# Optimization experiments

Hardware: AMD Instinct MI355X
Metric: run time of the kernel (lower is better)

The kernel has to match this reference:

```python
import jax, jax.numpy as jnp
import numpy as np

# alpha clamp limits: balance=False -> [exp(-1/5), exp(-1/25)]
ALPHA_MIN = float(np.exp(-1.0 / 5.0))
ALPHA_MAX = float(np.exp(-1.0 / 25.0))
T_CROP = 100


def setup_inputs() -> dict:
    key = jax.random.key(0)
    k1, k2, k3 = jax.random.split(key, 3)
    B, T, D, H = 128, 1000, 1024, 256
    x = jax.random.normal(k1, (B, T, D), dtype=jnp.float32)
    bound = float(np.sqrt(1.0 / D))
    W = jax.random.uniform(k2, (H, D), minval=-bound, maxval=bound, dtype=jnp.float32)
    alpha = jax.random.uniform(k3, (H,), minval=ALPHA_MIN, maxval=ALPHA_MAX, dtype=jnp.float32)
    return {"x": x, "W": W, "alpha": alpha}


def reference(x, W, alpha):
    # x: [B, T, D], W: [H, D], alpha: [H]
    a = jnp.clip(alpha, ALPHA_MIN, ALPHA_MAX)
    Wx = jnp.einsum('btd,hd->bth', x, W)  # [B, T, H]
    T = Wx.shape[1]
    mask = (jnp.arange(T) >= T_CROP).astype(Wx.dtype)  # [T]
    Wx_t = jnp.moveaxis(Wx, 1, 0)  # [T, B, H]

    def step(carry, inp):
        ut, out = carry
        wx, m = inp
        ut = a * ut + (1.0 - a) * wx
        out = out + m * jax.nn.softmax(ut, axis=-1)
        return (ut, out), None

    B, H = Wx.shape[0], Wx.shape[2]
    init = (jnp.zeros((B, H), Wx.dtype), jnp.zeros((B, H), Wx.dtype))
    (_, out), _ = jax.lax.scan(step, init, (Wx_t, mask))
    return out  # [B, H]
```

## Files before the change

### kernel.cpp

```cpp
#include <hip/hip_runtime.h>
#include <hip/hip_bf16.h>

#define B_    128
#define T_    1000
#define D_    1024
#define H_    256
#define TCROP 100
#define CHK   125
#define NC    8
#define NOUT  900

typedef __attribute__((ext_vector_type(8))) short bfrag8;
typedef __attribute__((ext_vector_type(4))) float f32x4;
typedef unsigned long long ull;

__device__ __forceinline__ unsigned short f2bf(float f) {
    union { float f; unsigned int u; } v; v.f = f;
    unsigned int u = v.u;
    u += 0x7FFFu + ((u >> 16) & 1u);
    return (unsigned short)(u >> 16);
}
__device__ __forceinline__ float bf2f(unsigned short u) {
    union { unsigned int u; float f; } v; v.u = ((unsigned int)u) << 16;
    return v.f;
}
__device__ __forceinline__ bfrag8 cvt8(float4 f0, float4 f1) {
    bfrag8 v;
    v[0] = (short)f2bf(f0.x); v[1] = (short)f2bf(f0.y);
    v[2] = (short)f2bf(f0.z); v[3] = (short)f2bf(f0.w);
    v[4] = (short)f2bf(f1.x); v[5] = (short)f2bf(f1.y);
    v[6] = (short)f2bf(f1.z); v[7] = (short)f2bf(f1.w);
    return v;
}

__global__ __launch_bounds__(256) void wconv_kernel(
        const float* __restrict__ W, unsigned short* __restrict__ Wbf) {
    const int i = (blockIdx.x * 256 + threadIdx.x) * 8;
    float4 f0 = *(const float4*)(W + i);
    float4 f1 = *(const float4*)(W + i + 4);
    *(bfrag8*)(Wbf + i) = cvt8(f0, f1);
}

__global__ __launch_bounds__(512) void gemm_ema_kernel(
        const float* __restrict__ x, const unsigned short* __restrict__ Wbf,
        const float* __restrict__ alpha,
        unsigned short* __restrict__ utl, float* __restrict__ F) {
    __shared__ unsigned short smem[128 * 256];
    unsigned short* As = smem;
    unsigned short* Bs = smem + 128 * 64;

    const int tid  = threadIdx.x;
    const int lane = tid & 63;
    const int wave = tid >> 6;
    const int wr   = wave >> 2;
    const int wc   = wave & 3;
    const int c    = blockIdx.x;
    const int b    = blockIdx.y;
    const int m0   = b * T_ + c * CHK;

    f32x4 acc[4][4];
#pragma unroll
    for (int m = 0; m < 4; ++m)
#pragma unroll
        for (int n = 0; n < 4; ++n) acc[m][n] = (f32x4){0.f, 0.f, 0.f, 0.f};

    const int rr  = lane & 15;
    const int kh  = lane >> 4;
    const int ra0 = tid >> 3;
    const int ja  = tid & 7;
    const int sa  = (ja ^ (ra0 & 7)) * 8;
    const int rA1 = (ra0 + 64 < CHK) ? (ra0 + 64) : (CHK - 1);
    const float* ap0 = x + (size_t)(m0 + ra0) * D_ + ja * 8;
    const float* ap1 = x + (size_t)(m0 + rA1) * D_ + ja * 8;

    float4 p00 = *(const float4*)ap0;
    float4 p01 = *(const float4*)(ap0 + 4);
    float4 p10 = *(const float4*)ap1;
    float4 p11 = *(const float4*)(ap1 + 4);

    for (int it = 0; it < 16; ++it) {
        const int kt = it * 64;
#pragma unroll
        for (int q = 0; q < 4; ++q) {
            const int li = q * 512 + tid;
            const int r = li >> 3, j = li & 7;
            const int jj = j ^ (r & 7);
            __builtin_amdgcn_global_load_lds(
                (const __attribute__((address_space(1))) void*)
                    (Wbf + (size_t)r * D_ + kt + jj * 8),
                (__attribute__((address_space(3))) void*)&Bs[li * 8], 16, 0, 0);
        }
        *(bfrag8*)&As[ra0 * 64 + sa]        = cvt8(p00, p01);
        *(bfrag8*)&As[(ra0 + 64) * 64 + sa] = cvt8(p10, p11);
        __syncthreads();
        if (it < 15) {
            const int ktn = kt + 64;
            p00 = *(const float4*)(ap0 + ktn);
            p01 = *(const float4*)(ap0 + ktn + 4);
            p10 = *(const float4*)(ap1 + ktn);
            p11 = *(const float4*)(ap1 + ktn + 4);
        }
#pragma unroll
        for (int kk = 0; kk < 2; ++kk) {
            const int c16 = kk * 4 + kh;
            bfrag8 af[4], bfr[4];
#pragma unroll
            for (int m = 0; m < 4; ++m) {
                const int row = wr * 64 + m * 16 + rr;
                af[m] = *(const bfrag8*)&As[row * 64 + ((c16 ^ (row & 7)) * 8)];
            }
#pragma unroll
            for (int n = 0; n < 4; ++n) {
                const int row = wc * 64 + n * 16 + rr;
                bfr[n] = *(const bfrag8*)&Bs[row * 64 + ((c16 ^ (row & 7)) * 8)];
            }
#pragma unroll
            for (int m = 0; m < 4; ++m)
#pragma unroll
                for (int n = 0; n < 4; ++n)
                    acc[m][n] = __builtin_amdgcn_mfma_f32_16x16x32_bf16(
                        af[m], bfr[n], acc[m][n], 0, 0, 0);
        }
        __syncthreads();
    }

    const int cl = lane & 15, rg = lane >> 4;
#pragma unroll
    for (int m = 0; m < 4; ++m)
#pragma unroll
        for (int n = 0; n < 4; ++n)
#pragma unroll
            for (int j = 0; j < 4; ++j) {
                const int row = wr * 64 + m * 16 + rg * 4 + j;
                const int col = (wc * 64 + n * 16 + cl + rg * 16) & 255;
                smem[row * 256 + col] = f2bf(acc[m][n][j]);
            }
    __syncthreads();

    if (tid < H_) {
        const int h = tid;
        const float AMIN = 0.81873075307798182f, AMAX = 0.96078943915232320f;
        const float a  = fminf(fmaxf(alpha[h], AMIN), AMAX);
        const float om = 1.0f - a;
        float ut = 0.f;
        const int t0 = c * CHK;
        for (int r = 0; r < CHK; ++r) {
            const int col = (h + ((r >> 2) & 3) * 16) & 255;
            ut = a * ut + om * bf2f(smem[r * 256 + col]);
            const int t = t0 + r;
            if (t >= TCROP)
                utl[((size_t)b * NOUT + (t - TCROP)) * H_ + h] = f2bf(ut);
        }
        F[((size_t)b * NC + c) * H_ + h] = ut;
    }
}

__global__ __launch_bounds__(64) void scanC_kernel(
        const unsigned short* __restrict__ utl, const float* __restrict__ alpha,
        const float* __restrict__ F, float* __restrict__ P) {
    const int c = blockIdx.x, b = blockIdx.y;
    const int lane = threadIdx.x;
    const int h4 = lane * 4;

    const float AMIN = 0.81873075307798182f, AMAX = 0.96078943915232320f;
    float4 al = *(const float4*)(alpha + h4);
    float a[4] = {fminf(fmaxf(al.x, AMIN), AMAX), fminf(fmaxf(al.y, AMIN), AMAX),
                  fminf(fmaxf(al.z, AMIN), AMAX), fminf(fmaxf(al.w, AMIN), AMAX)};

    float S[4] = {0.f, 0.f, 0.f, 0.f};
    if (c > 0) {
        float aL[4] = {__powf(a[0], (float)CHK), __powf(a[1], (float)CHK),
                       __powf(a[2], (float)CHK), __powf(a[3], (float)CHK)};
        for (int j = 0; j < c; ++j) {
            float4 f = *(const float4*)(F + ((size_t)b * NC + j) * H_ + h4);
            S[0] = aL[0] * S[0] + f.x;
            S[1] = aL[1] * S[1] + f.y;
            S[2] = aL[2] * S[2] + f.z;
            S[3] = aL[3] * S[3] + f.w;
        }
    }

    const int nt = (c == 0) ? (CHK - TCROP) : CHK;
    const size_t ti0 = (size_t)b * NOUT + (c == 0 ? 0 : c * CHK - TCROP);
    const unsigned short* base = utl + ti0 * H_ + h4;

    float d[4]    = {1.f, 1.f, 1.f, 1.f};
    float acc4[4] = {0.f, 0.f, 0.f, 0.f};

    for (int bb = 0; bb < nt; bb += 5) {
        float e[5][4], sl[5];
#pragma unroll
        for (int q = 0; q < 5; ++q) {
            ull wv = *(const ull*)(base + (size_t)(bb + q) * H_);
            d[0] *= a[0]; d[1] *= a[1]; d[2] *= a[2]; d[3] *= a[3];
            float u0 = bf2f((unsigned short)wv)         + d[0] * S[0];
            float u1 = bf2f((unsigned short)(wv >> 16)) + d[1] * S[1];
            float u2 = bf2f((unsigned short)(wv >> 32)) + d[2] * S[2];
            float u3 = bf2f((unsigned short)(wv >> 48)) + d[3] * S[3];
            e[q][0] = __expf(u0);
            e[q][1] = __expf(u1);
            e[q][2] = __expf(u2);
            e[q][3] = __expf(u3);
            sl[q] = (e[q][0] + e[q][1]) + (e[q][2] + e[q][3]);
        }
#pragma unroll
        for (int dd = 1; dd < 64; dd <<= 1) {
            sl[0] += __shfl_xor(sl[0], dd);
            sl[1] += __shfl_xor(sl[1], dd);
            sl[2] += __shfl_xor(sl[2], dd);
            sl[3] += __shfl_xor(sl[3], dd);
            sl[4] += __shfl_xor(sl[4], dd);
        }
#pragma unroll
        for (int q = 0; q < 5; ++q) {
            const float rcp = 1.0f / sl[q];
            acc4[0] += e[q][0] * rcp;
            acc4[1] += e[q][1] * rcp;
            acc4[2] += e[q][2] * rcp;
            acc4[3] += e[q][3] * rcp;
        }
    }
    float4 o; o.x = acc4[0]; o.y = acc4[1]; o.z = acc4[2]; o.w = acc4[3];
    *(float4*)(P + ((size_t)b * NC + c) * H_ + h4) = o;
}

__global__ __launch_bounds__(256) void scanD_kernel(
        const float* __restrict__ P, float* __restrict__ out) {
    const int b = blockIdx.x, h = threadIdx.x;
    float s = 0.f;
#pragma unroll
    for (int c = 0; c < NC; ++c) s += P[((size_t)b * NC + c) * H_ + h];
    out[(size_t)b * H_ + h] = s;
}

extern "C" void kernel_launch(void* const* d_in, const int* in_sizes, int n_in,
                              void* d_out, int out_size, void* d_ws, size_t ws_size,
                              hipStream_t stream) {
    const float* x     = (const float*)d_in[0];
    const float* W     = (const float*)d_in[1];
    const float* alpha = (const float*)d_in[2];
    float* out = (float*)d_out;

    char* ws = (char*)d_ws;
    unsigned short* Wbf = (unsigned short*)ws;
    unsigned short* utl = (unsigned short*)(ws + ((size_t)1 << 20));
    float* F = (float*)(ws + ((size_t)64 << 20));
    float* P = (float*)(ws + ((size_t)66 << 20));

    wconv_kernel<<<128, 256, 0, stream>>>(W, Wbf);
    gemm_ema_kernel<<<dim3(NC, B_), 512, 0, stream>>>(x, Wbf, alpha, utl, F);
    scanC_kernel<<<dim3(NC, B_), 64, 0, stream>>>(utl, alpha, F, P);
    scanD_kernel<<<B_, 256, 0, stream>>>(P, out);
}
```

Measured before the change: 205.3 us.

## Split GEMM from EMA scan and use finer 25-step chunks for scan parallelism

The GEMM no longer fuses the per-chunk EMA. It tiles the flattened B*T rows densely in 128-row blocks with no padded rows and writes Wx in bf16. Two new scan passes follow: one computes per-chunk EMA end states over 40 chunks of 25 steps, and one carries the prefix into each chunk, recomputing the EMA and summing softmax only for chunks past the crop. This spreads the serial recurrence across many more waves, at the cost of an extra Wx round trip and recomputing the EMA. The bf16 conversion also switches to a perm-based pack with round-half-up rounding.

```diff
diff --git a/kernel.cpp b/kernel.cpp
--- a/kernel.cpp
+++ b/kernel.cpp
@@ -6,9 +6,10 @@
 #define D_    1024
 #define H_    256
 #define TCROP 100
-#define CHK   125
-#define NC    8
-#define NOUT  900
+#define CHUNK 25
+#define NCHK  40
+#define CSKIP 4
+#define NOUTC 36
 
 typedef __attribute__((ext_vector_type(8))) short bfrag8;
 typedef __attribute__((ext_vector_type(4))) float f32x4;
@@ -24,13 +25,17 @@
     union { unsigned int u; float f; } v; v.u = ((unsigned int)u) << 16;
     return v.f;
 }
+__device__ __forceinline__ unsigned int pack2(float lo, float hi) {
+    union { float f; unsigned int u; } a, b; a.f = lo; b.f = hi;
+    return __builtin_amdgcn_perm(b.u + 0x8000u, a.u + 0x8000u, 0x07060302u);
+}
 __device__ __forceinline__ bfrag8 cvt8(float4 f0, float4 f1) {
-    bfrag8 v;
-    v[0] = (short)f2bf(f0.x); v[1] = (short)f2bf(f0.y);
-    v[2] = (short)f2bf(f0.z); v[3] = (short)f2bf(f0.w);
-    v[4] = (short)f2bf(f1.x); v[5] = (short)f2bf(f1.y);
-    v[6] = (short)f2bf(f1.z); v[7] = (short)f2bf(f1.w);
-    return v;
+    union { bfrag8 v; unsigned int u[4]; } r;
+    r.u[0] = pack2(f0.x, f0.y);
+    r.u[1] = pack2(f0.z, f0.w);
+    r.u[2] = pack2(f1.x, f1.y);
+    r.u[3] = pack2(f1.z, f1.w);
+    return r.v;
 }
 
 __global__ __launch_bounds__(256) void wconv_kernel(
@@ -41,22 +46,18 @@
     *(bfrag8*)(Wbf + i) = cvt8(f0, f1);
 }
 
-__global__ __launch_bounds__(512) void gemm_ema_kernel(
+__global__ __launch_bounds__(512, 4) void gemm_kernel(
         const float* __restrict__ x, const unsigned short* __restrict__ Wbf,
-        const float* __restrict__ alpha,
-        unsigned short* __restrict__ utl, float* __restrict__ F) {
-    __shared__ unsigned short smem[128 * 256];
-    unsigned short* As = smem;
-    unsigned short* Bs = smem + 128 * 64;
+        unsigned short* __restrict__ Wx) {
+    __shared__ unsigned short As[128 * 64];
+    __shared__ unsigned short Bs[256 * 64];
 
     const int tid  = threadIdx.x;
     const int lane = tid & 63;
     const int wave = tid >> 6;
     const int wr   = wave >> 2;
     const int wc   = wave & 3;
-    const int c    = blockIdx.x;
-    const int b    = blockIdx.y;
-    const int m0   = b * T_ + c * CHK;
+    const int m0   = blockIdx.x * 128;
 
     f32x4 acc[4][4];
 #pragma unroll
@@ -69,9 +70,8 @@
     const int ra0 = tid >> 3;
     const int ja  = tid & 7;
     const int sa  = (ja ^ (ra0 & 7)) * 8;
-    const int rA1 = (ra0 + 64 < CHK) ? (ra0 + 64) : (CHK - 1);
     const float* ap0 = x + (size_t)(m0 + ra0) * D_ + ja * 8;
-    const float* ap1 = x + (size_t)(m0 + rA1) * D_ + ja * 8;
+    const float* ap1 = ap0 + (size_t)64 * D_;
 
     float4 p00 = *(const float4*)ap0;
     float4 p01 = *(const float4*)(ap0 + 4);
@@ -131,76 +131,85 @@
         for (int n = 0; n < 4; ++n)
 #pragma unroll
             for (int j = 0; j < 4; ++j) {
-                const int row = wr * 64 + m * 16 + rg * 4 + j;
-                const int col = (wc * 64 + n * 16 + cl + rg * 16) & 255;
-                smem[row * 256 + col] = f2bf(acc[m][n][j]);
+                const int row = m0 + wr * 64 + m * 16 + rg * 4 + j;
+                const int col = wc * 64 + n * 16 + cl;
+                Wx[(size_t)row * H_ + col] = f2bf(acc[m][n][j]);
             }
-    __syncthreads();
-
-    if (tid < H_) {
-        const int h = tid;
-        const float AMIN = 0.81873075307798182f, AMAX = 0.96078943915232320f;
-        const float a  = fminf(fmaxf(alpha[h], AMIN), AMAX);
-        const float om = 1.0f - a;
-        float ut = 0.f;
-        const int t0 = c * CHK;
-        for (int r = 0; r < CHK; ++r) {
-            const int col = (h + ((r >> 2) & 3) * 16) & 255;
-            ut = a * ut + om * bf2f(smem[r * 256 + col]);
-            const int t = t0 + r;
-            if (t >= TCROP)
-                utl[((size_t)b * NOUT + (t - TCROP)) * H_ + h] = f2bf(ut);
-        }
-        F[((size_t)b * NC + c) * H_ + h] = ut;
-    }
-}
-
-__global__ __launch_bounds__(64) void scanC_kernel(
-        const unsigned short* __restrict__ utl, const float* __restrict__ alpha,
-        const float* __restrict__ F, float* __restrict__ P) {
-    const int c = blockIdx.x, b = blockIdx.y;
-    const int lane = threadIdx.x;
+}
+
+__global__ __launch_bounds__(256) void scanA_kernel(
+        const unsigned short* __restrict__ Wx, const float* __restrict__ alpha,
+        float* __restrict__ F) {
+    const int wave = threadIdx.x >> 6;
+    const int lane = threadIdx.x & 63;
+    const int c = blockIdx.x * 4 + wave;
+    const int b = blockIdx.y;
     const int h4 = lane * 4;
 
     const float AMIN = 0.81873075307798182f, AMAX = 0.96078943915232320f;
     float4 al = *(const float4*)(alpha + h4);
-    float a[4] = {fminf(fmaxf(al.x, AMIN), AMAX), fminf(fmaxf(al.y, AMIN), AMAX),
-                  fminf(fmaxf(al.z, AMIN), AMAX), fminf(fmaxf(al.w, AMIN), AMAX)};
-
+    float a[4]  = {fminf(fmaxf(al.x, AMIN), AMAX), fminf(fmaxf(al.y, AMIN), AMAX),
+                   fminf(fmaxf(al.z, AMIN), AMAX), fminf(fmaxf(al.w, AMIN), AMAX)};
+    float om[4] = {1.f - a[0], 1.f - a[1], 1.f - a[2], 1.f - a[3]};
+
+    float ut[4] = {0.f, 0.f, 0.f, 0.f};
+    const unsigned short* base = Wx + ((size_t)b * T_ + c * CHUNK) * H_ + h4;
+#pragma unroll 5
+    for (int t = 0; t < CHUNK; ++t) {
+        ull wv = *(const ull*)(base + (size_t)t * H_);
+        ut[0] = a[0] * ut[0] + om[0] * bf2f((unsigned short)wv);
+        ut[1] = a[1] * ut[1] + om[1] * bf2f((unsigned short)(wv >> 16));
+        ut[2] = a[2] * ut[2] + om[2] * bf2f((unsigned short)(wv >> 32));
+        ut[3] = a[3] * ut[3] + om[3] * bf2f((unsigned short)(wv >> 48));
+    }
+    float4 o; o.x = ut[0]; o.y = ut[1]; o.z = ut[2]; o.w = ut[3];
+    *(float4*)(F + ((size_t)b * NCHK + c) * H_ + h4) = o;
+}
+
+__global__ __launch_bounds__(256) void scanC_kernel(
+        const unsigned short* __restrict__ Wx, const float* __restrict__ alpha,
+        const float* __restrict__ F, float* __restrict__ P) {
+    const int wave = threadIdx.x >> 6;
+    const int lane = threadIdx.x & 63;
+    const int c = CSKIP + blockIdx.x * 4 + wave;
+    const int b = blockIdx.y;
+    const int h4 = lane * 4;
+
+    const float AMIN = 0.81873075307798182f, AMAX = 0.96078943915232320f;
+    float4 al = *(const float4*)(alpha + h4);
+    float a[4]  = {fminf(fmaxf(al.x, AMIN), AMAX), fminf(fmaxf(al.y, AMIN), AMAX),
+                   fminf(fmaxf(al.z, AMIN), AMAX), fminf(fmaxf(al.w, AMIN), AMAX)};
+    float om[4] = {1.f - a[0], 1.f - a[1], 1.f - a[2], 1.f - a[3]};
+
+    float aL[4] = {__powf(a[0], (float)CHUNK), __powf(a[1], (float)CHUNK),
+                   __powf(a[2], (float)CHUNK), __powf(a[3], (float)CHUNK)};
     float S[4] = {0.f, 0.f, 0.f, 0.f};
-    if (c > 0) {
-        float aL[4] = {__powf(a[0], (float)CHK), __powf(a[1], (float)CHK),
-                       __powf(a[2], (float)CHK), __powf(a[3], (float)CHK)};
-        for (int j = 0; j < c; ++j) {
-            float4 f = *(const float4*)(F + ((size_t)b * NC + j) * H_ + h4);
-            S[0] = aL[0] * S[0] + f.x;
-            S[1] = aL[1] * S[1] + f.y;
-            S[2] = aL[2] * S[2] + f.z;
-            S[3] = aL[3] * S[3] + f.w;
-        }
-    }
-
-    const int nt = (c == 0) ? (CHK - TCROP) : CHK;
-    const size_t ti0 = (size_t)b * NOUT + (c == 0 ? 0 : c * CHK - TCROP);
-    const unsigned short* base = utl + ti0 * H_ + h4;
-
-    float d[4]    = {1.f, 1.f, 1.f, 1.f};
+    for (int j = 0; j < c; ++j) {
+        float4 f = *(const float4*)(F + ((size_t)b * NCHK + j) * H_ + h4);
+        S[0] = aL[0] * S[0] + f.x;
+        S[1] = aL[1] * S[1] + f.y;
+        S[2] = aL[2] * S[2] + f.z;
+        S[3] = aL[3] * S[3] + f.w;
+    }
+
+    float ut[4]   = {S[0], S[1], S[2], S[3]};
     float acc4[4] = {0.f, 0.f, 0.f, 0.f};
-
-    for (int bb = 0; bb < nt; bb += 5) {
+    const unsigned short* base = Wx + ((size_t)b * T_ + c * CHUNK) * H_ + h4;
+
+#pragma unroll
+    for (int bb = 0; bb < CHUNK; bb += 5) {
         float e[5][4], sl[5];
 #pragma unroll
         for (int q = 0; q < 5; ++q) {
             ull wv = *(const ull*)(base + (size_t)(bb + q) * H_);
-            d[0] *= a[0]; d[1] *= a[1]; d[2] *= a[2]; d[3] *= a[3];
-            float u0 = bf2f((unsigned short)wv)         + d[0] * S[0];
-            float u1 = bf2f((unsigned short)(wv >> 16)) + d[1] * S[1];
-            float u2 = bf2f((unsigned short)(wv >> 32)) + d[2] * S[2];
-            float u3 = bf2f((unsigned short)(wv >> 48)) + d[3] * S[3];
-            e[q][0] = __expf(u0);
-            e[q][1] = __expf(u1);
-            e[q][2] = __expf(u2);
-            e[q][3] = __expf(u3);
+            ut[0] = a[0] * ut[0] + om[0] * bf2f((unsigned short)wv);
+            ut[1] = a[1] * ut[1] + om[1] * bf2f((unsigned short)(wv >> 16));
+            ut[2] = a[2] * ut[2] + om[2] * bf2f((unsigned short)(wv >> 32));
+            ut[3] = a[3] * ut[3] + om[3] * bf2f((unsigned short)(wv >> 48));
+            e[q][0] = __expf(ut[0]);
+            e[q][1] = __expf(ut[1]);
+            e[q][2] = __expf(ut[2]);
+            e[q][3] = __expf(ut[3]);
             sl[q] = (e[q][0] + e[q][1]) + (e[q][2] + e[q][3]);
         }
 #pragma unroll
@@ -221,15 +230,15 @@
         }
     }
     float4 o; o.x = acc4[0]; o.y = acc4[1]; o.z = acc4[2]; o.w = acc4[3];
-    *(float4*)(P + ((size_t)b * NC + c) * H_ + h4) = o;
+    *(float4*)(P + ((size_t)b * NOUTC + (c - CSKIP)) * H_ + h4) = o;
 }
 
 __global__ __launch_bounds__(256) void scanD_kernel(
         const float* __restrict__ P, float* __restrict__ out) {
     const int b = blockIdx.x, h = threadIdx.x;
     float s = 0.f;
-#pragma unroll
-    for (int c = 0; c < NC; ++c) s += P[((size_t)b * NC + c) * H_ + h];
+#pragma unroll 4
+    for (int k = 0; k < NOUTC; ++k) s += P[((size_t)b * NOUTC + k) * H_ + h];
     out[(size_t)b * H_ + h] = s;
 }
 
@@ -243,12 +252,13 @@
 
     char* ws = (char*)d_ws;
     unsigned short* Wbf = (unsigned short*)ws;
-    unsigned short* utl = (unsigned short*)(ws + ((size_t)1 << 20));
-    float* F = (float*)(ws + ((size_t)64 << 20));
-    float* P = (float*)(ws + ((size_t)66 << 20));
+    unsigned short* Wx  = (unsigned short*)(ws + ((size_t)1 << 20));
+    float* F = (float*)(ws + ((size_t)70 << 20));
+    float* P = (float*)(ws + ((size_t)80 << 20));
 
     wconv_kernel<<<128, 256, 0, stream>>>(W, Wbf);
-    gemm_ema_kernel<<<dim3(NC, B_), 512, 0, stream>>>(x, Wbf, alpha, utl, F);
-    scanC_kernel<<<dim3(NC, B_), 64, 0, stream>>>(utl, alpha, F, P);
+    gemm_kernel<<<(B_ * T_) / 128, 512, 0, stream>>>(x, Wbf, Wx);
+    scanA_kernel<<<dim3(NCHK / 4, B_), 256, 0, stream>>>(Wx, alpha, F);
+    scanC_kernel<<<dim3(NOUTC / 4, B_), 256, 0, stream>>>(Wx, alpha, F, P);
     scanD_kernel<<<B_, 256, 0, stream>>>(P, out);
 }
```

Result: faster. 194.9 us (-5.1%).
